# Kernel optimization log

Hardware: AMD Instinct MI355X
Metric: run time of the kernel (lower is better)

Reference implementation:

```python
import jax, jax.numpy as jnp
import numpy as np

N, E = 50000, 800000
IN_F, HID, HEADS, OUT_F = 128, 32, 4, 40
SLOPE = 0.2  # LeakyReLU negative slope (alpha)


def gatv2_layer(x, Wl, Wr, att, src, dst, n):
    # GATv2 (Brody et al.): score_ij = att . leakyrelu(Wl x_j + Wr x_i), message = Wl x_j
    H, F = att.shape
    gl = (x @ Wl).reshape(n, H, F)  # [N,H,F] source transform
    gr = (x @ Wr).reshape(n, H, F)  # [N,H,F] dest transform
    s = gl[src] + gr[dst]           # [E,H,F]
    e = jnp.where(s > 0, s, SLOPE * s)
    score = jnp.einsum('ehf,hf->eh', e, att)  # [E,H]
    m = jax.lax.stop_gradient(jax.ops.segment_max(score, dst, num_segments=n))
    a = jnp.exp(score - m[dst])
    denom = jax.ops.segment_sum(a, dst, num_segments=n)  # [N,H]
    w = a / (denom[dst] + 1e-16)                          # softmax over incoming edges
    out = jax.ops.segment_sum(w[:, :, None] * gl[src], dst, num_segments=n)  # [N,H,F]
    return out.reshape(n, H * F)


def setup_inputs() -> dict:
    key = jax.random.key(0)
    ks = jax.random.split(key, 12)
    d1 = HEADS * HID  # 128
    sc_in = 1.0 / np.sqrt(IN_F)
    sc_h = 1.0 / np.sqrt(d1)
    return {
        'x': jax.random.normal(ks[0], (N, IN_F), jnp.float32),
        'Wl1': jax.random.normal(ks[1], (IN_F, d1), jnp.float32) * sc_in,
        'Wr1': jax.random.normal(ks[2], (IN_F, d1), jnp.float32) * sc_in,
        'att1': jax.random.normal(ks[3], (HEADS, HID), jnp.float32) * (1.0 / np.sqrt(HID)),
        'Wl2': jax.random.normal(ks[4], (d1, d1), jnp.float32) * sc_h,
        'Wr2': jax.random.normal(ks[5], (d1, d1), jnp.float32) * sc_h,
        'att2': jax.random.normal(ks[6], (HEADS, HID), jnp.float32) * (1.0 / np.sqrt(HID)),
        'Wl3': jax.random.normal(ks[7], (d1, OUT_F), jnp.float32) * sc_h,
        'Wr3': jax.random.normal(ks[8], (d1, OUT_F), jnp.float32) * sc_h,
        'att3': jax.random.normal(ks[9], (1, OUT_F), jnp.float32) * (1.0 / np.sqrt(OUT_F)),
        'edge_index': jax.random.randint(ks[10], (2, E), 0, N, jnp.int64 if jax.config.jax_enable_x64 else jnp.int32),
    }


def reference(x, Wl1, Wr1, att1, Wl2, Wr2, att2, Wl3, Wr3, att3, edge_index):
    src, dst = edge_index[0], edge_index[1]
    h = jax.nn.elu(gatv2_layer(x, Wl1, Wr1, att1, src, dst, N))        # conv1 + ELU
    h = jax.nn.relu(gatv2_layer(h, Wl2, Wr2, att2, src, dst, N))       # hidden + ReLU (dropout off: eval)
    h = gatv2_layer(h, Wl3, Wr3, att3, src, dst, N)                    # conv2, 1 head
    return jax.nn.log_softmax(h, axis=1)
```

## Files before the change

kernel.cpp:

```cpp
#include <hip/hip_runtime.h>
#include <math.h>


#define TPB 256

typedef __attribute__((ext_vector_type(8))) short short8v;
typedef __attribute__((ext_vector_type(4))) float f32x4;

__device__ __forceinline__ short bf16rne(float v, float* recon) {
  unsigned u = __float_as_uint(v);
  unsigned r = (u + 0x7FFFu + ((u >> 16) & 1u)) >> 16;
  if (recon) *recon = __uint_as_float(r << 16);
  return (short)r;
}
__device__ __forceinline__ float bf2f(unsigned short u) {
  return __uint_as_float((unsigned)u << 16);
}

__global__ void k_prepW6(const float* __restrict__ s0, const float* __restrict__ s1,
                         const float* __restrict__ s2, const float* __restrict__ s3,
                         const float* __restrict__ s4, const float* __restrict__ s5,
                         short* __restrict__ wt) {
  int y = blockIdx.y;
  const float* W; short* hi; int M, Mp;
  if (y < 4) {
    W = (y == 0) ? s0 : (y == 1) ? s1 : (y == 2) ? s2 : s3;
    hi = wt + y * 32768; M = 128; Mp = 128;
  } else {
    W = (y == 4) ? s4 : s5;
    hi = wt + 131072 + (y - 4) * 12288; M = 40; Mp = 48;
  }
  short* lo = hi + 128 * Mp;
  int t = blockIdx.x * blockDim.x + threadIdx.x;
  if (t >= 128 * Mp) return;
  int m = t % Mp, k = t / Mp;
  float v = (m < M) ? W[k * M + m] : 0.f;
  float vh;
  short h = bf16rne(v, &vh);
  short l = bf16rne(v - vh, nullptr);
  hi[(size_t)m * 128 + k] = h;
  lo[(size_t)m * 128 + k] = l;
}

template <int ACT>
__device__ __forceinline__ void loadA(const float* __restrict__ x, int arow, int koff,
                                      short8v AH[4], short8v AL[4]) {
  const float4* px = reinterpret_cast<const float4*>(x + (size_t)arow * 128 + koff);
  float4 t[8];
#pragma unroll
  for (int k = 0; k < 4; ++k) {
    t[2 * k]     = px[k * 8];
    t[2 * k + 1] = px[k * 8 + 1];
  }
#pragma unroll
  for (int k = 0; k < 4; ++k) {
    float av[8] = {t[2 * k].x, t[2 * k].y, t[2 * k].z, t[2 * k].w,
                   t[2 * k + 1].x, t[2 * k + 1].y, t[2 * k + 1].z, t[2 * k + 1].w};
#pragma unroll
    for (int j = 0; j < 8; ++j) {
      float v = av[j];
      if (ACT == 1) v = v > 0.f ? v : (__expf(v) - 1.f);
      else if (ACT == 2) v = fmaxf(v, 0.f);
      float vh;
      AH[k][j] = bf16rne(v, &vh);
      AL[k][j] = bf16rne(v - vh, nullptr);
    }
  }
}

template <int ACT>
__global__ __launch_bounds__(256) void k_gemm_mfma(
    const float* __restrict__ x,
    const short* __restrict__ blh, const short* __restrict__ bll,
    const short* __restrict__ brh, const short* __restrict__ brl,
    unsigned short* __restrict__ glh, float* __restrict__ gr, int n) {
  const int K = 128;
  int lane = threadIdx.x & 63;
  int w = threadIdx.x >> 6;
  int rbase = blockIdx.x * 16;
  int arow = rbase + (lane & 15);
  if (arow >= n) arow = n - 1;
  int koff = (lane >> 4) * 8;

  short8v AH[4], AL[4];
  loadA<ACT>(x, arow, koff, AH, AL);

  f32x4 acc[2][2];
#pragma unroll
  for (int m = 0; m < 2; ++m)
#pragma unroll
    for (int c = 0; c < 2; ++c) acc[m][c] = (f32x4)(0.f);

  int bbase = (lane & 15) * K + koff;
  const int cb = w * 2;

#define BOFF(IT) (((cb + ((IT) & 1)) * 16 * K) + bbase + (((IT) >> 1) * 32))
  short8v cbh = *reinterpret_cast<const short8v*>(blh + BOFF(0));
  short8v cbl = *reinterpret_cast<const short8v*>(bll + BOFF(0));
  short8v cch = *reinterpret_cast<const short8v*>(brh + BOFF(0));
  short8v ccl = *reinterpret_cast<const short8v*>(brl + BOFF(0));
#pragma unroll
  for (int it = 0; it < 8; ++it) {
    const int k0i = it >> 1, ci = it & 1;
    const int nit = (it + 1) & 7;
    short8v nbh = *reinterpret_cast<const short8v*>(blh + BOFF(nit));
    short8v nbl = *reinterpret_cast<const short8v*>(bll + BOFF(nit));
    short8v nch = *reinterpret_cast<const short8v*>(brh + BOFF(nit));
    short8v ncl = *reinterpret_cast<const short8v*>(brl + BOFF(nit));
    acc[0][ci] = __builtin_amdgcn_mfma_f32_16x16x32_bf16(AH[k0i], cbh, acc[0][ci], 0, 0, 0);
    acc[0][ci] = __builtin_amdgcn_mfma_f32_16x16x32_bf16(AH[k0i], cbl, acc[0][ci], 0, 0, 0);
    acc[0][ci] = __builtin_amdgcn_mfma_f32_16x16x32_bf16(AL[k0i], cbh, acc[0][ci], 0, 0, 0);
    acc[1][ci] = __builtin_amdgcn_mfma_f32_16x16x32_bf16(AH[k0i], cch, acc[1][ci], 0, 0, 0);
    acc[1][ci] = __builtin_amdgcn_mfma_f32_16x16x32_bf16(AH[k0i], ccl, acc[1][ci], 0, 0, 0);
    acc[1][ci] = __builtin_amdgcn_mfma_f32_16x16x32_bf16(AL[k0i], cch, acc[1][ci], 0, 0, 0);
    cbh = nbh; cbl = nbl; cch = nch; ccl = ncl;
  }
#undef BOFF

  int crow = rbase + (lane >> 4) * 4;
  int ccol = lane & 15;
#pragma unroll
  for (int ci = 0; ci < 2; ++ci) {
    int c = cb + ci;
#pragma unroll
    for (int j = 0; j < 4; ++j) {
      int r = crow + j;
      if (r < n) {
        glh[(size_t)r * 128 + c * 16 + ccol] = (unsigned short)bf16rne(acc[0][ci][j], nullptr);
        gr[(size_t)r * 128 + c * 16 + ccol] = acc[1][ci][j];
      }
    }
  }
}

template <int ACT>
__global__ __launch_bounds__(192) void k_gemm_mfma3(
    const float* __restrict__ x,
    const short* __restrict__ blh, const short* __restrict__ bll,
    const short* __restrict__ brh, const short* __restrict__ brl,
    unsigned short* __restrict__ glh, float* __restrict__ gr, int n) {
  const int K = 128;
  int lane = threadIdx.x & 63;
  int w = threadIdx.x >> 6;
  int rbase = blockIdx.x * 16;
  int arow = rbase + (lane & 15);
  if (arow >= n) arow = n - 1;
  int koff = (lane >> 4) * 8;

  short8v AH[4], AL[4];
  loadA<ACT>(x, arow, koff, AH, AL);

  int bbase = w * 16 * K + (lane & 15) * K + koff;

  short8v Bh[4], Bl[4], Ch[4], Cl[4];
#pragma unroll
  for (int k = 0; k < 4; ++k) {
    Bh[k] = *reinterpret_cast<const short8v*>(blh + bbase + k * 32);
    Bl[k] = *reinterpret_cast<const short8v*>(bll + bbase + k * 32);
    Ch[k] = *reinterpret_cast<const short8v*>(brh + bbase + k * 32);
    Cl[k] = *reinterpret_cast<const short8v*>(brl + bbase + k * 32);
  }

  f32x4 accL = (f32x4)(0.f), accR = (f32x4)(0.f);
#pragma unroll
  for (int k = 0; k < 4; ++k) {
    accL = __builtin_amdgcn_mfma_f32_16x16x32_bf16(AH[k], Bh[k], accL, 0, 0, 0);
    accL = __builtin_amdgcn_mfma_f32_16x16x32_bf16(AH[k], Bl[k], accL, 0, 0, 0);
    accL = __builtin_amdgcn_mfma_f32_16x16x32_bf16(AL[k], Bh[k], accL, 0, 0, 0);
    accR = __builtin_amdgcn_mfma_f32_16x16x32_bf16(AH[k], Ch[k], accR, 0, 0, 0);
    accR = __builtin_amdgcn_mfma_f32_16x16x32_bf16(AH[k], Cl[k], accR, 0, 0, 0);
    accR = __builtin_amdgcn_mfma_f32_16x16x32_bf16(AL[k], Ch[k], accR, 0, 0, 0);
  }

  int crow = rbase + (lane >> 4) * 4;
  int ccol = lane & 15;
  int col = w * 16 + ccol;
#pragma unroll
  for (int j = 0; j < 4; ++j) {
    int r = crow + j;
    if (r < n && col < 40) {
      glh[(size_t)r * 40 + col] = (unsigned short)bf16rne(accL[j], nullptr);
      gr[(size_t)r * 40 + col] = accR[j];
    }
  }
}

__global__ void k_hist(const int* __restrict__ dst, int* __restrict__ cnt, int E) {
  int e = blockIdx.x * blockDim.x + threadIdx.x;
  if (e < E) atomicAdd(&cnt[dst[e]], 1);
}

__global__ void k_scan1(const int* __restrict__ cnt, int* __restrict__ rowptr,
                        int* __restrict__ bsum, int n) {
  __shared__ int wsum[16];
  int i = blockIdx.x * 1024 + threadIdx.x;
  int lane = threadIdx.x & 63, wid = threadIdx.x >> 6;
  int v = (i < n) ? cnt[i] : 0;
  int x = v;
#pragma unroll
  for (int off = 1; off < 64; off <<= 1) {
    int t = __shfl_up(x, off);
    if (lane >= off) x += t;
  }
  if (lane == 63) wsum[wid] = x;
  __syncthreads();
  if (wid == 0) {
    int wv = (lane < 16) ? wsum[lane] : 0;
#pragma unroll
    for (int off = 1; off < 16; off <<= 1) {
      int t = __shfl_up(wv, off);
      if (lane >= off) wv += t;
    }
    if (lane < 16) wsum[lane] = wv;
  }
  __syncthreads();
  int woff = wid ? wsum[wid - 1] : 0;
  if (i < n) rowptr[i] = woff + x - v;
  if (threadIdx.x == 1023) bsum[blockIdx.x] = wsum[15];
}

__global__ void k_scan2(const int* __restrict__ bsum, int* __restrict__ boff, int nb,
                        int* __restrict__ rowptr, int n) {
  int lane = threadIdx.x;
  int v = (lane < nb) ? bsum[lane] : 0;
  int x = v;
#pragma unroll
  for (int off = 1; off < 64; off <<= 1) {
    int t = __shfl_up(x, off);
    if (lane >= off) x += t;
  }
  if (lane < nb) boff[lane] = x - v;
  if (lane == 63) rowptr[n] = x;
}

__global__ void k_scan3(int* __restrict__ rowptr, const int* __restrict__ boff,
                        int* __restrict__ cur, int n) {
  int i = blockIdx.x * blockDim.x + threadIdx.x;
  if (i < n) {
    int r = rowptr[i] + boff[i >> 10];
    rowptr[i] = r;
    cur[i] = r;
  }
}

__global__ void k_fill(const int* __restrict__ src, const int* __restrict__ dst,
                       int* __restrict__ cur, int* __restrict__ csr_src, int E) {
  int e = blockIdx.x * blockDim.x + threadIdx.x;
  if (e >= E) return;
  int pos = atomicAdd(&cur[dst[e]], 1);
  csr_src[pos] = src[e];
}

__global__ void k_edge4(const unsigned short* __restrict__ glh, const float* __restrict__ gr,
                        const float* __restrict__ att, const int* __restrict__ rowptr,
                        const int* __restrict__ csr_src, float* __restrict__ out, int n) {
  int wid = (int)((blockIdx.x * blockDim.x + threadIdx.x) >> 6);
  if (wid >= n) return;
  int lane = threadIdx.x & 63;
  int p0 = rowptr[wid], p1 = rowptr[wid + 1];
  float2* po = reinterpret_cast<float2*>(out + (size_t)wid * 128);
  if (p1 <= p0) { po[lane] = make_float2(0.f, 0.f); return; }
  const float2 grv = reinterpret_cast<const float2*>(gr + (size_t)wid * 128)[lane];
  const float2 attv = reinterpret_cast<const float2*>(att)[lane];

  float l[8];
  float2 acc[8];
#pragma unroll
  for (int j = 0; j < 8; ++j) { l[j] = 0.f; acc[j] = make_float2(0.f, 0.f); }

#define LD(S) ({ ushort2 u_ = reinterpret_cast<const ushort2*>(glh + ((size_t)(S) << 7))[lane]; \
                 make_float2(bf2f(u_.x), bf2f(u_.y)); })
#define UPD4(J, G)                                                     \
  {                                                                    \
    float vx = (G).x + grv.x; vx = vx > 0.f ? vx : 0.2f * vx;          \
    float vy = (G).y + grv.y; vy = vy > 0.f ? vy : 0.2f * vy;          \
    float part = fmaf(vx, attv.x, vy * attv.y);                        \
    part += __shfl_xor(part, 1);                                       \
    part += __shfl_xor(part, 2);                                       \
    part += __shfl_xor(part, 4);                                       \
    part += __shfl_xor(part, 8);                                       \
    float w = __expf(part);                                            \
    l[J] += w;                                                         \
    acc[J].x = fmaf(w, (G).x, acc[J].x);                               \
    acc[J].y = fmaf(w, (G).y, acc[J].y);                               \
  }

  for (int base = p0; base < p1; base += 64) {
    int nv = p1 - base; if (nv > 64) nv = 64;
    int sv = (base + lane < p1) ? csr_src[base + lane] : 0;
    int i = 0;
    for (; i + 8 <= nv; i += 8) {
      int s0 = __shfl(sv, i + 0), s1 = __shfl(sv, i + 1);
      int s2 = __shfl(sv, i + 2), s3 = __shfl(sv, i + 3);
      int s4 = __shfl(sv, i + 4), s5 = __shfl(sv, i + 5);
      int s6 = __shfl(sv, i + 6), s7 = __shfl(sv, i + 7);
      float2 g0 = LD(s0), g1 = LD(s1), g2 = LD(s2), g3 = LD(s3);
      float2 g4 = LD(s4), g5 = LD(s5), g6 = LD(s6), g7 = LD(s7);
      UPD4(0, g0); UPD4(1, g1); UPD4(2, g2); UPD4(3, g3);
      UPD4(4, g4); UPD4(5, g5); UPD4(6, g6); UPD4(7, g7);
    }
    for (; i < nv; ++i) {
      int s0 = __shfl(sv, i);
      float2 g0 = LD(s0);
      UPD4(0, g0);
    }
  }
#undef UPD4
#undef LD

  float lt = 0.f;
  float2 at = make_float2(0.f, 0.f);
#pragma unroll
  for (int j = 0; j < 8; ++j) {
    lt += l[j];
    at.x += acc[j].x;
    at.y += acc[j].y;
  }
  float inv = 1.f / (lt + 1e-16f);
  po[lane] = make_float2(at.x * inv, at.y * inv);
}

__global__ void k_edge1ls(const unsigned short* __restrict__ glh, const float* __restrict__ gr,
                          const float* __restrict__ att, const int* __restrict__ rowptr,
                          const int* __restrict__ csr_src, float* __restrict__ outf, int n) {
  int wv = (int)((blockIdx.x * blockDim.x + threadIdx.x) >> 6);
  int lane = threadIdx.x & 63;
  int half = lane >> 5, hl = lane & 31;
  int d = wv * 2 + half;
  if (d >= n) d = n - 1;
  bool fok = hl < 20;
  float2 grv = fok ? reinterpret_cast<const float2*>(gr + (size_t)d * 40)[hl]
                   : make_float2(0.f, 0.f);
  float2 attv = fok ? reinterpret_cast<const float2*>(att)[hl] : make_float2(0.f, 0.f);
  int p0 = rowptr[d], p1 = rowptr[d + 1];
  int ec = p1 - p0;
  int nch = (ec + 31) >> 5;
  { int o = __shfl_xor(nch, 32); nch = nch > o ? nch : o; }

  float l0 = 0.f, l1 = 0.f;
  float2 a0 = make_float2(0.f, 0.f), a1 = make_float2(0.f, 0.f);

  for (int c = 0; c < nch; ++c) {
    int base = p0 + c * 32;
    int sv = (base + hl < p1) ? csr_src[base + hl] : 0;
    int nv = p1 - base;
    nv = nv < 0 ? 0 : (nv > 32 ? 32 : nv);
    int nvmax = nv;
    { int o = __shfl_xor(nvmax, 32); nvmax = nvmax > o ? nvmax : o; }
    for (int i = 0; i < nvmax; i += 2) {
      int s0 = __shfl(sv, (half << 5) + i);
      int s1 = __shfl(sv, (half << 5) + i + 1);
      bool v0 = i < nv, v1 = (i + 1) < nv;
      float2 g0 = make_float2(0.f, 0.f), g1 = make_float2(0.f, 0.f);
      if (v0 && fok) { ushort2 u = reinterpret_cast<const ushort2*>(glh + (size_t)s0 * 40)[hl]; g0 = make_float2(bf2f(u.x), bf2f(u.y)); }
      if (v1 && fok) { ushort2 u = reinterpret_cast<const ushort2*>(glh + (size_t)s1 * 40)[hl]; g1 = make_float2(bf2f(u.x), bf2f(u.y)); }
      float e0x = g0.x + grv.x; e0x = e0x > 0.f ? e0x : 0.2f * e0x;
      float e0y = g0.y + grv.y; e0y = e0y > 0.f ? e0y : 0.2f * e0y;
      float pt0 = fmaf(e0x, attv.x, e0y * attv.y);
      float e1x = g1.x + grv.x; e1x = e1x > 0.f ? e1x : 0.2f * e1x;
      float e1y = g1.y + grv.y; e1y = e1y > 0.f ? e1y : 0.2f * e1y;
      float pt1 = fmaf(e1x, attv.x, e1y * attv.y);
#pragma unroll
      for (int o = 1; o < 32; o <<= 1) {
        pt0 += __shfl_xor(pt0, o);
        pt1 += __shfl_xor(pt1, o);
      }
      float w0 = v0 ? __expf(pt0) : 0.f;
      float w1 = v1 ? __expf(pt1) : 0.f;
      l0 += w0;
      a0.x = fmaf(w0, g0.x, a0.x);
      a0.y = fmaf(w0, g0.y, a0.y);
      l1 += w1;
      a1.x = fmaf(w1, g1.x, a1.x);
      a1.y = fmaf(w1, g1.y, a1.y);
    }
  }

  float lt = l0 + l1;
  float inv = 1.f / (lt + 1e-16f);
  float ox = (a0.x + a1.x) * inv;
  float oy = (a0.y + a1.y) * inv;

  float mx = fok ? fmaxf(ox, oy) : -INFINITY;
#pragma unroll
  for (int o = 1; o < 32; o <<= 1) mx = fmaxf(mx, __shfl_xor(mx, o));
  float ex = fok ? (__expf(ox - mx) + __expf(oy - mx)) : 0.f;
  float sm = ex;
#pragma unroll
  for (int o = 1; o < 32; o <<= 1) sm += __shfl_xor(sm, o);
  float lg = logf(sm);
  if (fok) {
    float2* po = reinterpret_cast<float2*>(outf + (size_t)d * 40);
    po[hl] = make_float2(ox - mx - lg, oy - mx - lg);
  }
}

static inline int cdiv(long long a, int b) { return (int)((a + b - 1) / b); }

extern "C" void kernel_launch(void* const* d_in, const int* in_sizes, int n_in,
                              void* d_out, int out_size, void* d_ws, size_t ws_size,
                              hipStream_t stream) {
  const float* x    = (const float*)d_in[0];
  const float* Wl1  = (const float*)d_in[1];
  const float* Wr1  = (const float*)d_in[2];
  const float* att1 = (const float*)d_in[3];
  const float* Wl2  = (const float*)d_in[4];
  const float* Wr2  = (const float*)d_in[5];
  const float* att2 = (const float*)d_in[6];
  const float* Wl3  = (const float*)d_in[7];
  const float* Wr3  = (const float*)d_in[8];
  const float* att3 = (const float*)d_in[9];
  const int*   ei   = (const int*)d_in[10];

  const int N = in_sizes[0] / 128;
  const int E = in_sizes[10] / 2;
  const int* src = ei;
  const int* dst = ei + E;

  short* wt = (short*)d_ws;
  short* wl1h = wt +      0;  short* wl1l = wt +  16384;
  short* wr1h = wt +  32768;  short* wr1l = wt +  49152;
  short* wl2h = wt +  65536;  short* wl2l = wt +  81920;
  short* wr2h = wt +  98304;  short* wr2l = wt + 114688;
  short* wl3h = wt + 131072;  short* wl3l = wt + 137216;
  short* wr3h = wt + 143360;  short* wr3l = wt + 149504;

  float* fbase  = (float*)d_ws + 77824;
  float* bufA   = fbase;
  float* bufGR  = bufA + (size_t)N * 128;
  unsigned short* bufGLh = (unsigned short*)(bufGR + (size_t)N * 128);
  int*   cnt    = (int*)(bufGR + (size_t)N * 128 + (size_t)N * 64);
  int*   rowptr = cnt + N;
  int*   cur    = rowptr + N + 1;
  int*   csrS   = cur + N;
  int*   bsum   = csrS + E;
  int*   boff   = bsum + 64;

  float* outf = (float*)d_out;

  const int nb = cdiv(N, 1024);

  hipMemsetAsync(cnt, 0, (size_t)N * sizeof(int), stream);
  k_hist<<<cdiv(E, TPB), TPB, 0, stream>>>(dst, cnt, E);
  k_prepW6<<<dim3(64, 6), TPB, 0, stream>>>(Wl1, Wr1, Wl2, Wr2, Wl3, Wr3, wt);
  k_scan1<<<nb, 1024, 0, stream>>>(cnt, rowptr, bsum, N);
  k_scan2<<<1, 64, 0, stream>>>(bsum, boff, nb, rowptr, N);
  k_scan3<<<cdiv(N, TPB), TPB, 0, stream>>>(rowptr, boff, cur, N);
  k_fill<<<cdiv(E, TPB), TPB, 0, stream>>>(src, dst, cur, csrS, E);

  k_gemm_mfma<0><<<cdiv(N, 16), 256, 0, stream>>>(x, wl1h, wl1l, wr1h, wr1l, bufGLh, bufGR, N);
  k_edge4<<<cdiv(N, 4), TPB, 0, stream>>>(bufGLh, bufGR, att1, rowptr, csrS, bufA, N);

  k_gemm_mfma<1><<<cdiv(N, 16), 256, 0, stream>>>(bufA, wl2h, wl2l, wr2h, wr2l, bufGLh, bufGR, N);
  k_edge4<<<cdiv(N, 4), TPB, 0, stream>>>(bufGLh, bufGR, att2, rowptr, csrS, bufA, N);

  k_gemm_mfma3<2><<<cdiv(N, 16), 192, 0, stream>>>(bufA, wl3h, wl3l, wr3h, wr3l, bufGLh, bufGR, N);
  k_edge1ls<<<cdiv(cdiv(N, 2), 4), TPB, 0, stream>>>(bufGLh, bufGR, att3, rowptr, csrS, outf, N);
}
```

Measured before the change: 507.1 us.

## Move activation and bf16 hi/lo split into edge kernel epilogue

The ELU/ReLU activation and the split of GEMM inputs into bf16 high and low parts now happen in the aggregation kernel's epilogue, and in a new pre-pass for x, instead of inside every GEMM block's load. The GEMMs then read ready-made bf16 hi/lo operands, each 2 bytes per element (4 bytes per value for the pair, the same as fp32). This removes the per-tile conversion arithmetic, and exp work, from the GEMM kernels. It adds an extra kernel launch and a full read and write pass over x.

```diff
diff --git a/kernel.cpp b/kernel.cpp
--- a/kernel.cpp
+++ b/kernel.cpp
@@ -15,6 +15,24 @@
 }
 __device__ __forceinline__ float bf2f(unsigned short u) {
   return __uint_as_float((unsigned)u << 16);
+}
+
+__global__ void k_prepX(const float* __restrict__ x, unsigned short* __restrict__ ah,
+                        unsigned short* __restrict__ al, int total8) {
+  int t = blockIdx.x * blockDim.x + threadIdx.x;
+  if (t >= total8) return;
+  const float4* px = reinterpret_cast<const float4*>(x) + (size_t)t * 2;
+  float4 a = px[0], b = px[1];
+  float av[8] = {a.x, a.y, a.z, a.w, b.x, b.y, b.z, b.w};
+  short8v h, l;
+#pragma unroll
+  for (int j = 0; j < 8; ++j) {
+    float vh;
+    h[j] = bf16rne(av[j], &vh);
+    l[j] = bf16rne(av[j] - vh, nullptr);
+  }
+  *reinterpret_cast<short8v*>(ah + (size_t)t * 8) = h;
+  *reinterpret_cast<short8v*>(al + (size_t)t * 8) = l;
 }
 
 __global__ void k_prepW6(const float* __restrict__ s0, const float* __restrict__ s1,
@@ -42,35 +60,8 @@
   lo[(size_t)m * 128 + k] = l;
 }
 
-template <int ACT>
-__device__ __forceinline__ void loadA(const float* __restrict__ x, int arow, int koff,
-                                      short8v AH[4], short8v AL[4]) {
-  const float4* px = reinterpret_cast<const float4*>(x + (size_t)arow * 128 + koff);
-  float4 t[8];
-#pragma unroll
-  for (int k = 0; k < 4; ++k) {
-    t[2 * k]     = px[k * 8];
-    t[2 * k + 1] = px[k * 8 + 1];
-  }
-#pragma unroll
-  for (int k = 0; k < 4; ++k) {
-    float av[8] = {t[2 * k].x, t[2 * k].y, t[2 * k].z, t[2 * k].w,
-                   t[2 * k + 1].x, t[2 * k + 1].y, t[2 * k + 1].z, t[2 * k + 1].w};
-#pragma unroll
-    for (int j = 0; j < 8; ++j) {
-      float v = av[j];
-      if (ACT == 1) v = v > 0.f ? v : (__expf(v) - 1.f);
-      else if (ACT == 2) v = fmaxf(v, 0.f);
-      float vh;
-      AH[k][j] = bf16rne(v, &vh);
-      AL[k][j] = bf16rne(v - vh, nullptr);
-    }
-  }
-}
-
-template <int ACT>
 __global__ __launch_bounds__(256) void k_gemm_mfma(
-    const float* __restrict__ x,
+    const unsigned short* __restrict__ ah, const unsigned short* __restrict__ al,
     const short* __restrict__ blh, const short* __restrict__ bll,
     const short* __restrict__ brh, const short* __restrict__ brl,
     unsigned short* __restrict__ glh, float* __restrict__ gr, int n) {
@@ -83,7 +74,11 @@
   int koff = (lane >> 4) * 8;
 
   short8v AH[4], AL[4];
-  loadA<ACT>(x, arow, koff, AH, AL);
+#pragma unroll
+  for (int k = 0; k < 4; ++k) {
+    AH[k] = *reinterpret_cast<const short8v*>(ah + (size_t)arow * 128 + k * 32 + koff);
+    AL[k] = *reinterpret_cast<const short8v*>(al + (size_t)arow * 128 + k * 32 + koff);
+  }
 
   f32x4 acc[2][2];
 #pragma unroll
@@ -133,9 +128,8 @@
   }
 }
 
-template <int ACT>
 __global__ __launch_bounds__(192) void k_gemm_mfma3(
-    const float* __restrict__ x,
+    const unsigned short* __restrict__ ah, const unsigned short* __restrict__ al,
     const short* __restrict__ blh, const short* __restrict__ bll,
     const short* __restrict__ brh, const short* __restrict__ brl,
     unsigned short* __restrict__ glh, float* __restrict__ gr, int n) {
@@ -148,7 +142,11 @@
   int koff = (lane >> 4) * 8;
 
   short8v AH[4], AL[4];
-  loadA<ACT>(x, arow, koff, AH, AL);
+#pragma unroll
+  for (int k = 0; k < 4; ++k) {
+    AH[k] = *reinterpret_cast<const short8v*>(ah + (size_t)arow * 128 + k * 32 + koff);
+    AL[k] = *reinterpret_cast<const short8v*>(al + (size_t)arow * 128 + k * 32 + koff);
+  }
 
   int bbase = w * 16 * K + (lane & 15) * K + koff;
 
@@ -251,15 +249,19 @@
   csr_src[pos] = src[e];
 }
 
+template <int ACTOUT>
 __global__ void k_edge4(const unsigned short* __restrict__ glh, const float* __restrict__ gr,
                         const float* __restrict__ att, const int* __restrict__ rowptr,
-                        const int* __restrict__ csr_src, float* __restrict__ out, int n) {
+                        const int* __restrict__ csr_src,
+                        unsigned short* __restrict__ oah, unsigned short* __restrict__ oal,
+                        int n) {
   int wid = (int)((blockIdx.x * blockDim.x + threadIdx.x) >> 6);
   if (wid >= n) return;
   int lane = threadIdx.x & 63;
   int p0 = rowptr[wid], p1 = rowptr[wid + 1];
-  float2* po = reinterpret_cast<float2*>(out + (size_t)wid * 128);
-  if (p1 <= p0) { po[lane] = make_float2(0.f, 0.f); return; }
+  ushort2* pah = reinterpret_cast<ushort2*>(oah + (size_t)wid * 128) + lane;
+  ushort2* pal = reinterpret_cast<ushort2*>(oal + (size_t)wid * 128) + lane;
+  if (p1 <= p0) { *pah = make_ushort2(0, 0); *pal = make_ushort2(0, 0); return; }
   const float2 grv = reinterpret_cast<const float2*>(gr + (size_t)wid * 128)[lane];
   const float2 attv = reinterpret_cast<const float2*>(att)[lane];
 
@@ -317,7 +319,21 @@
     at.y += acc[j].y;
   }
   float inv = 1.f / (lt + 1e-16f);
-  po[lane] = make_float2(at.x * inv, at.y * inv);
+  float ox = at.x * inv, oy = at.y * inv;
+  if (ACTOUT == 1) {
+    ox = ox > 0.f ? ox : (__expf(ox) - 1.f);
+    oy = oy > 0.f ? oy : (__expf(oy) - 1.f);
+  } else {
+    ox = fmaxf(ox, 0.f);
+    oy = fmaxf(oy, 0.f);
+  }
+  float rx, ry;
+  unsigned short hx = (unsigned short)bf16rne(ox, &rx);
+  unsigned short hy = (unsigned short)bf16rne(oy, &ry);
+  unsigned short lx = (unsigned short)bf16rne(ox - rx, nullptr);
+  unsigned short ly = (unsigned short)bf16rne(oy - ry, nullptr);
+  *pah = make_ushort2(hx, hy);
+  *pal = make_ushort2(lx, ly);
 }
 
 __global__ void k_edge1ls(const unsigned short* __restrict__ glh, const float* __restrict__ gr,
@@ -425,11 +441,11 @@
   short* wl3h = wt + 131072;  short* wl3l = wt + 137216;
   short* wr3h = wt + 143360;  short* wr3l = wt + 149504;
 
-  float* fbase  = (float*)d_ws + 77824;
-  float* bufA   = fbase;
-  float* bufGR  = bufA + (size_t)N * 128;
-  unsigned short* bufGLh = (unsigned short*)(bufGR + (size_t)N * 128);
-  int*   cnt    = (int*)(bufGR + (size_t)N * 128 + (size_t)N * 64);
+  unsigned short* ah  = (unsigned short*)(wt + 155648);
+  unsigned short* al  = ah + (size_t)N * 128;
+  float* bufGR        = (float*)(al + (size_t)N * 128);
+  unsigned short* glh = (unsigned short*)(bufGR + (size_t)N * 128);
+  int*   cnt    = (int*)(glh + (size_t)N * 128);
   int*   rowptr = cnt + N;
   int*   cur    = rowptr + N + 1;
   int*   csrS   = cur + N;
@@ -443,17 +459,18 @@
   hipMemsetAsync(cnt, 0, (size_t)N * sizeof(int), stream);
   k_hist<<<cdiv(E, TPB), TPB, 0, stream>>>(dst, cnt, E);
   k_prepW6<<<dim3(64, 6), TPB, 0, stream>>>(Wl1, Wr1, Wl2, Wr2, Wl3, Wr3, wt);
+  k_prepX<<<cdiv((long long)N * 16, TPB), TPB, 0, stream>>>(x, ah, al, N * 16);
   k_scan1<<<nb, 1024, 0, stream>>>(cnt, rowptr, bsum, N);
   k_scan2<<<1, 64, 0, stream>>>(bsum, boff, nb, rowptr, N);
   k_scan3<<<cdiv(N, TPB), TPB, 0, stream>>>(rowptr, boff, cur, N);
   k_fill<<<cdiv(E, TPB), TPB, 0, stream>>>(src, dst, cur, csrS, E);
 
-  k_gemm_mfma<0><<<cdiv(N, 16), 256, 0, stream>>>(x, wl1h, wl1l, wr1h, wr1l, bufGLh, bufGR, N);
-  k_edge4<<<cdiv(N, 4), TPB, 0, stream>>>(bufGLh, bufGR, att1, rowptr, csrS, bufA, N);
-
-  k_gemm_mfma<1><<<cdiv(N, 16), 256, 0, stream>>>(bufA, wl2h, wl2l, wr2h, wr2l, bufGLh, bufGR, N);
-  k_edge4<<<cdiv(N, 4), TPB, 0, stream>>>(bufGLh, bufGR, att2, rowptr, csrS, bufA, N);
-
-  k_gemm_mfma3<2><<<cdiv(N, 16), 192, 0, stream>>>(bufA, wl3h, wl3l, wr3h, wr3l, bufGLh, bufGR, N);
-  k_edge1ls<<<cdiv(cdiv(N, 2), 4), TPB, 0, stream>>>(bufGLh, bufGR, att3, rowptr, csrS, outf, N);
-}
+  k_gemm_mfma<<<cdiv(N, 16), 256, 0, stream>>>(ah, al, wl1h, wl1l, wr1h, wr1l, glh, bufGR, N);
+  k_edge4<1><<<cdiv(N, 4), TPB, 0, stream>>>(glh, bufGR, att1, rowptr, csrS, ah, al, N);
+
+  k_gemm_mfma<<<cdiv(N, 16), 256, 0, stream>>>(ah, al, wl2h, wl2l, wr2h, wr2l, glh, bufGR, N);
+  k_edge4<2><<<cdiv(N, 4), TPB, 0, stream>>>(glh, bufGR, att2, rowptr, csrS, ah, al, N);
+
+  k_gemm_mfma3<<<cdiv(N, 16), 192, 0, stream>>>(ah, al, wl3h, wl3l, wr3h, wr3l, glh, bufGR, N);
+  k_edge1ls<<<cdiv(cdiv(N, 2), 4), TPB, 0, stream>>>(glh, bufGR, att3, rowptr, csrS, outf, N);
+}
```

After: 509.7 us. No clear change (+0.5%).
